# Kernel tuning notes

Measured on AMD Instinct MI355X. Metric: run time of the kernel, lower is better.

Reference implementation:

```python
import jax, jax.numpy as jnp
import numpy as np

EPS = 1e-06
BASE = 1.414  # warp_exponent_base


def _forward_splat(vals, flow_x, flow_y):
    """Differentiable forward warp (bilinear splatting / scatter-add).

    vals:   [B, K, H, W] source values to splat
    flow_x: [B, H, W]    horizontal flow (target_x = x + flow_x)
    flow_y: [B, H, W]    vertical flow
    returns [B, K, H, W]
    """
    B, K, H, W = vals.shape
    N = B * H * W
    xs = jnp.arange(W, dtype=vals.dtype)
    ys = jnp.arange(H, dtype=vals.dtype)
    tx = xs[None, None, :] + flow_x            # [B,H,W]
    ty = ys[None, :, None] + flow_y
    x0f = jnp.floor(tx)
    y0f = jnp.floor(ty)
    wx1 = tx - x0f
    wx0 = 1.0 - wx1
    wy1 = ty - y0f
    wy0 = 1.0 - wy1
    x0 = x0f.astype(jnp.int32)
    y0 = y0f.astype(jnp.int32)
    x1 = x0 + 1
    y1 = y0 + 1

    boff = (jnp.arange(B, dtype=jnp.int32) * (H * W))[:, None, None]  # [B,1,1]
    v = vals.transpose(0, 2, 3, 1).reshape(N, K)  # [N,K] source pixel values

    out = jnp.zeros((N, K), dtype=vals.dtype)
    for xi, yi, w in ((x0, y0, wx0 * wy0), (x1, y0, wx1 * wy0),
                      (x0, y1, wx0 * wy1), (x1, y1, wx1 * wy1)):
        valid = (xi >= 0) & (xi < W) & (yi >= 0) & (yi < H)
        idx = boff + yi * W + xi                       # [B,H,W]
        idx = jnp.where(valid, idx, N).reshape(N)      # OOB -> dropped
        out = out.at[idx].add(v * w.reshape(N, 1), mode='drop')
    return out.reshape(B, H, W, K).transpose(0, 3, 1, 2)


def setup_inputs() -> dict:
    key = jax.random.key(0)
    k1, k2 = jax.random.split(key)
    B, C, H, W = 16, 3, 512, 960
    im = jax.random.uniform(k1, (B, C, H, W), dtype=jnp.float32)
    disp = jax.random.uniform(k2, (B, 1, H, W), dtype=jnp.float32) * 40.0
    return {"im": im, "disp": disp}


def reference(im, disp):
    # convergence = 0.0 (default)
    wmap = jnp.power(jnp.float32(BASE), disp - disp.min())   # [B,1,H,W]
    flow_x = -disp[:, 0]                                     # [B,H,W]
    flow_y = jnp.zeros_like(flow_x)
    C = im.shape[1]
    # Fuse the three fw() calls (im*wmap, wmap, ones) into one multi-channel splat.
    chans = jnp.concatenate([im * wmap, wmap, jnp.ones_like(wmap)], axis=1)
    splat = _forward_splat(chans, flow_x, flow_y)
    res_accum = splat[:, :C]
    mask = jnp.maximum(splat[:, C:C + 1], EPS)
    res = res_accum / mask
    occ = 1.0 - jnp.clip(splat[:, C + 1:C + 2], 0.0, 1.0)
    return res, occ
```

## Files before the change

### kernel.cpp

```cpp
#include <hip/hip_runtime.h>
#include <math.h>

#define B_ 16
#define C_ 3
#define H_ 512
#define W_ 960
constexpr int HW = H_ * W_;
constexpr float EPS_ = 1e-6f;
constexpr float LOG2_BASE = 0.49978213f;

typedef __attribute__((ext_vector_type(2))) float f2;

__global__ __launch_bounds__(256) void splat_kernel(const float* __restrict__ im,
                                                    const float* __restrict__ disp,
                                                    float* __restrict__ out) {
    __shared__ float  txS[4 * 257];
    __shared__ float4 fS [4 * 257];

    const int row = blockIdx.x;
    const int b   = row >> 9;
    const int y   = row & (H_ - 1);
    const int rowoff = row * W_;
    const float* imr = im + (size_t)b * C_ * HW + (size_t)y * W_;
    const int tid = threadIdx.x;

    for (int i = tid; i < 4 * 257; i += 256) {
        float txv = -1.0e9f;
        float4 f  = make_float4(0.f, 0.f, 0.f, 0.f);
        if (i < W_) {
            float d = disp[rowoff + i];
            float w = exp2f(d * LOG2_BASE);
            txv = (float)i - d;
            f = make_float4(imr[i] * w, imr[HW + i] * w, imr[2 * HW + i] * w, w);
        }
        txS[(i & 3) * 257 + (i >> 2)] = txv;
        fS [(i & 3) * 257 + (i >> 2)] = f;
    }
    __syncthreads();

    if (tid < 240) {
        const float t0 = (float)(4 * tid);
        f2 A0a = 0.f, A0b = 0.f, A1a = 0.f, A1b = 0.f, A2a = 0.f, A2b = 0.f;
        f2 AWa = 0.f, AWb = 0.f, ACa = 0.f, ACb = 0.f;
        const f2 OFFa = {0.0f, 1.0f};
        const f2 OFFb = {2.0f, 3.0f};

        #pragma unroll
        for (int p = 0; p < 4; ++p) {
            const float*  txrow = &txS[p * 257 + tid];
            const float4* frow  = &fS [p * 257 + tid];
            const int cmax = (p == 0) ? 12 : 11;
            #pragma unroll
            for (int c = 0; c < cmax; ++c) {
                float  txv = txrow[c];
                float4 f   = frow[c];
                float d0 = txv - t0;
                f2 ea = d0 - OFFa;
                f2 eb = d0 - OFFb;
                f2 wa, wb;
                wa.x = __builtin_fmaxf(1.0f - __builtin_fabsf(ea.x), 0.0f);
                wa.y = __builtin_fmaxf(1.0f - __builtin_fabsf(ea.y), 0.0f);
                wb.x = __builtin_fmaxf(1.0f - __builtin_fabsf(eb.x), 0.0f);
                wb.y = __builtin_fmaxf(1.0f - __builtin_fabsf(eb.y), 0.0f);
                A0a += f.x * wa;  A0b += f.x * wb;
                A1a += f.y * wa;  A1b += f.y * wb;
                A2a += f.z * wa;  A2b += f.z * wb;
                AWa += f.w * wa;  AWb += f.w * wb;
                ACa += wa;        ACb += wb;
            }
        }

        float i0 = __builtin_amdgcn_rcpf(__builtin_fmaxf(AWa.x, EPS_));
        float i1 = __builtin_amdgcn_rcpf(__builtin_fmaxf(AWa.y, EPS_));
        float i2 = __builtin_amdgcn_rcpf(__builtin_fmaxf(AWb.x, EPS_));
        float i3 = __builtin_amdgcn_rcpf(__builtin_fmaxf(AWb.y, EPS_));
        float4 r0 = make_float4(A0a.x * i0, A0a.y * i1, A0b.x * i2, A0b.y * i3);
        float4 r1 = make_float4(A1a.x * i0, A1a.y * i1, A1b.x * i2, A1b.y * i3);
        float4 r2 = make_float4(A2a.x * i0, A2a.y * i1, A2b.x * i2, A2b.y * i3);
        float4 oc = make_float4(1.0f - __builtin_fminf(ACa.x, 1.0f),
                                1.0f - __builtin_fminf(ACa.y, 1.0f),
                                1.0f - __builtin_fminf(ACb.x, 1.0f),
                                1.0f - __builtin_fminf(ACb.y, 1.0f));

        float* o0 = out + (size_t)b * C_ * HW + (size_t)y * W_ + 4 * tid;
        *(float4*)(o0)          = r0;
        *(float4*)(o0 + HW)     = r1;
        *(float4*)(o0 + 2 * HW) = r2;
        *(float4*)(out + (size_t)B_ * C_ * HW + (size_t)rowoff + 4 * tid) = oc;
    }
}

extern "C" void kernel_launch(void* const* d_in, const int* in_sizes, int n_in,
                              void* d_out, int out_size, void* d_ws, size_t ws_size,
                              hipStream_t stream) {
    const float* im   = (const float*)d_in[0];
    const float* disp = (const float*)d_in[1];
    float* out        = (float*)d_out;

    splat_kernel<<<B_ * H_, 256, 0, stream>>>(im, disp, out);
}
```

Measured before the change: 234.3 us.

## Compute eight outputs per thread with 8-phase LDS layout and vectorized staging

```diff
diff --git a/kernel.cpp b/kernel.cpp
--- a/kernel.cpp
+++ b/kernel.cpp
@@ -10,12 +10,14 @@
 constexpr float LOG2_BASE = 0.49978213f;
 
 typedef __attribute__((ext_vector_type(2))) float f2;
+typedef __attribute__((ext_vector_type(4))) float f4v;
 
-__global__ __launch_bounds__(256) void splat_kernel(const float* __restrict__ im,
-                                                    const float* __restrict__ disp,
-                                                    float* __restrict__ out) {
-    __shared__ float  txS[4 * 257];
-    __shared__ float4 fS [4 * 257];
+__global__ __launch_bounds__(128, 4) void splat_kernel(const float* __restrict__ im,
+                                                       const float* __restrict__ disp,
+                                                       float* __restrict__ out) {
+    constexpr int SLOTS = 125;
+    __shared__ float  txS[8 * SLOTS];
+    __shared__ float4 fS [8 * SLOTS];
 
     const int row = blockIdx.x;
     const int b   = row >> 9;
@@ -24,78 +26,99 @@
     const float* imr = im + (size_t)b * C_ * HW + (size_t)y * W_;
     const int tid = threadIdx.x;
 
-    for (int i = tid; i < 4 * 257; i += 256) {
-        float txv = -1.0e9f;
-        float4 f  = make_float4(0.f, 0.f, 0.f, 0.f);
-        if (i < W_) {
-            float d = disp[rowoff + i];
+    if (tid < 40) {
+        const int p = tid / 5, s = 120 + tid % 5;
+        txS[p * SLOTS + s] = -1.0e9f;
+        fS [p * SLOTS + s] = make_float4(0.f, 0.f, 0.f, 0.f);
+    }
+
+    for (int i = tid; i < 240; i += 128) {
+        const int x0 = 4 * i;
+        f4v d4 = *(const f4v*)(disp + rowoff + x0);
+        f4v c0 = *(const f4v*)(imr + x0);
+        f4v c1 = *(const f4v*)(imr + HW + x0);
+        f4v c2 = *(const f4v*)(imr + 2 * HW + x0);
+        #pragma unroll
+        for (int k = 0; k < 4; ++k) {
+            const int x = x0 + k;
+            const int p = x & 7, s = x >> 3;
+            float d = d4[k];
             float w = exp2f(d * LOG2_BASE);
-            txv = (float)i - d;
-            f = make_float4(imr[i] * w, imr[HW + i] * w, imr[2 * HW + i] * w, w);
+            txS[p * SLOTS + s] = (float)x - d;
+            fS [p * SLOTS + s] = make_float4(c0[k] * w, c1[k] * w, c2[k] * w, w);
         }
-        txS[(i & 3) * 257 + (i >> 2)] = txv;
-        fS [(i & 3) * 257 + (i >> 2)] = f;
     }
     __syncthreads();
 
-    if (tid < 240) {
-        const float t0 = (float)(4 * tid);
-        f2 A0a = 0.f, A0b = 0.f, A1a = 0.f, A1b = 0.f, A2a = 0.f, A2b = 0.f;
-        f2 AWa = 0.f, AWb = 0.f, ACa = 0.f, ACb = 0.f;
-        const f2 OFFa = {0.0f, 1.0f};
-        const f2 OFFb = {2.0f, 3.0f};
+    if (tid >= 120) return;
 
+    const float t0 = (float)(8 * tid);
+    f2 T0[4], A0[4], A1[4], A2[4], AW[4], AC[4];
+    #pragma unroll
+    for (int q = 0; q < 4; ++q) {
+        T0[q] = (f2){t0 + (float)(2 * q), t0 + (float)(2 * q + 1)};
+        A0[q] = 0.f; A1[q] = 0.f; A2[q] = 0.f; AW[q] = 0.f; AC[q] = 0.f;
+    }
+
+    #pragma unroll
+    for (int p = 0; p < 8; ++p) {
+        const float*  txrow = &txS[p * SLOTS + tid];
+        const float4* frow  = &fS [p * SLOTS + tid];
         #pragma unroll
-        for (int p = 0; p < 4; ++p) {
-            const float*  txrow = &txS[p * 257 + tid];
-            const float4* frow  = &fS [p * 257 + tid];
-            const int cmax = (p == 0) ? 12 : 11;
+        for (int c = 0; c < 6; ++c) {
+            float  txv = txrow[c];
+            float4 f   = frow[c];
+            const f2 txv2 = {txv, txv};
             #pragma unroll
-            for (int c = 0; c < cmax; ++c) {
-                float  txv = txrow[c];
-                float4 f   = frow[c];
-                float d0 = txv - t0;
-                f2 ea = d0 - OFFa;
-                f2 eb = d0 - OFFb;
-                f2 wa, wb;
-                wa.x = __builtin_fmaxf(1.0f - __builtin_fabsf(ea.x), 0.0f);
-                wa.y = __builtin_fmaxf(1.0f - __builtin_fabsf(ea.y), 0.0f);
-                wb.x = __builtin_fmaxf(1.0f - __builtin_fabsf(eb.x), 0.0f);
-                wb.y = __builtin_fmaxf(1.0f - __builtin_fabsf(eb.y), 0.0f);
-                A0a += f.x * wa;  A0b += f.x * wb;
-                A1a += f.y * wa;  A1b += f.y * wb;
-                A2a += f.z * wa;  A2b += f.z * wb;
-                AWa += f.w * wa;  AWb += f.w * wb;
-                ACa += wa;        ACb += wb;
+            for (int q = 0; q < 4; ++q) {
+                f2 e = txv2 - T0[q];
+                f2 w;
+                w.x = __builtin_fmaxf(1.0f - __builtin_fabsf(e.x), 0.0f);
+                w.y = __builtin_fmaxf(1.0f - __builtin_fabsf(e.y), 0.0f);
+                A0[q] += f.x * w;
+                A1[q] += f.y * w;
+                A2[q] += f.z * w;
+                AW[q] += f.w * w;
+                AC[q] += w;
             }
         }
+    }
 
-        float i0 = __builtin_amdgcn_rcpf(__builtin_fmaxf(AWa.x, EPS_));
-        float i1 = __builtin_amdgcn_rcpf(__builtin_fmaxf(AWa.y, EPS_));
-        float i2 = __builtin_amdgcn_rcpf(__builtin_fmaxf(AWb.x, EPS_));
-        float i3 = __builtin_amdgcn_rcpf(__builtin_fmaxf(AWb.y, EPS_));
-        float4 r0 = make_float4(A0a.x * i0, A0a.y * i1, A0b.x * i2, A0b.y * i3);
-        float4 r1 = make_float4(A1a.x * i0, A1a.y * i1, A1b.x * i2, A1b.y * i3);
-        float4 r2 = make_float4(A2a.x * i0, A2a.y * i1, A2b.x * i2, A2b.y * i3);
-        float4 oc = make_float4(1.0f - __builtin_fminf(ACa.x, 1.0f),
-                                1.0f - __builtin_fminf(ACa.y, 1.0f),
-                                1.0f - __builtin_fminf(ACb.x, 1.0f),
-                                1.0f - __builtin_fminf(ACb.y, 1.0f));
+    float i0 = __builtin_amdgcn_rcpf(__builtin_fmaxf(AW[0].x, EPS_));
+    float i1 = __builtin_amdgcn_rcpf(__builtin_fmaxf(AW[0].y, EPS_));
+    float i2 = __builtin_amdgcn_rcpf(__builtin_fmaxf(AW[1].x, EPS_));
+    float i3 = __builtin_amdgcn_rcpf(__builtin_fmaxf(AW[1].y, EPS_));
+    float i4 = __builtin_amdgcn_rcpf(__builtin_fmaxf(AW[2].x, EPS_));
+    float i5 = __builtin_amdgcn_rcpf(__builtin_fmaxf(AW[2].y, EPS_));
+    float i6 = __builtin_amdgcn_rcpf(__builtin_fmaxf(AW[3].x, EPS_));
+    float i7 = __builtin_amdgcn_rcpf(__builtin_fmaxf(AW[3].y, EPS_));
 
-        float* o0 = out + (size_t)b * C_ * HW + (size_t)y * W_ + 4 * tid;
-        *(float4*)(o0)          = r0;
-        *(float4*)(o0 + HW)     = r1;
-        *(float4*)(o0 + 2 * HW) = r2;
-        *(float4*)(out + (size_t)B_ * C_ * HW + (size_t)rowoff + 4 * tid) = oc;
-    }
+    float* o0 = out + (size_t)b * C_ * HW + (size_t)y * W_ + 8 * tid;
+    *(float4*)(o0)              = make_float4(A0[0].x * i0, A0[0].y * i1, A0[1].x * i2, A0[1].y * i3);
+    *(float4*)(o0 + 4)          = make_float4(A0[2].x * i4, A0[2].y * i5, A0[3].x * i6, A0[3].y * i7);
+    *(float4*)(o0 + HW)         = make_float4(A1[0].x * i0, A1[0].y * i1, A1[1].x * i2, A1[1].y * i3);
+    *(float4*)(o0 + HW + 4)     = make_float4(A1[2].x * i4, A1[2].y * i5, A1[3].x * i6, A1[3].y * i7);
+    *(float4*)(o0 + 2 * HW)     = make_float4(A2[0].x * i0, A2[0].y * i1, A2[1].x * i2, A2[1].y * i3);
+    *(float4*)(o0 + 2 * HW + 4) = make_float4(A2[2].x * i4, A2[2].y * i5, A2[3].x * i6, A2[3].y * i7);
+
+    float* oc = out + (size_t)B_ * C_ * HW + (size_t)rowoff + 8 * tid;
+    *(float4*)(oc)     = make_float4(1.0f - __builtin_fminf(AC[0].x, 1.0f),
+                                     1.0f - __builtin_fminf(AC[0].y, 1.0f),
+                                     1.0f - __builtin_fminf(AC[1].x, 1.0f),
+                                     1.0f - __builtin_fminf(AC[1].y, 1.0f));
+    *(float4*)(oc + 4) = make_float4(1.0f - __builtin_fminf(AC[2].x, 1.0f),
+                                     1.0f - __builtin_fminf(AC[2].y, 1.0f),
+                                     1.0f - __builtin_fminf(AC[3].x, 1.0f),
+                                     1.0f - __builtin_fminf(AC[3].y, 1.0f));
 }
 
 extern "C" void kernel_launch(void* const* d_in, const int* in_sizes, int n_in,
                               void* d_out, int out_size, void* d_ws, size_t ws_size,
                               hipStream_t stream) {
+    (void)in_sizes; (void)n_in; (void)out_size; (void)d_ws; (void)ws_size;
     const float* im   = (const float*)d_in[0];
     const float* disp = (const float*)d_in[1];
     float* out        = (float*)d_out;
 
-    splat_kernel<<<B_ * H_, 256, 0, stream>>>(im, disp, out);
+    splat_kernel<<<B_ * H_, 128, 0, stream>>>(im, disp, out);
 }
```

Measured after the change: 231.6 us. No clear change (-1.1%).
